# Performance work log

Hardware: AMD Instinct MI355X
Metric: run time of the kernel (lower is better)

The kernel has to match this reference:

```python
import jax, jax.numpy as jnp
import numpy as np

D = 1024      # n_embd
H = 16        # n_head
HD = D // H   # head_size = 64


def _layernorm(x, g, b, eps=1e-5):
    mu = jnp.mean(x, axis=-1, keepdims=True)
    var = jnp.mean((x - mu) ** 2, axis=-1, keepdims=True)
    return (x - mu) * jax.lax.rsqrt(var + eps) * g + b


def setup_inputs() -> dict:
    key = jax.random.key(0)
    ks = jax.random.split(key, 12)
    s = lambda fan_in: 1.0 / np.sqrt(fan_in)
    inp = {
        "x": jax.random.normal(ks[0], (4, 2048, D), dtype=jnp.float32),
        # attention projections (bias=False in Head), per-head weights fused into [D, D]
        "wq": jax.random.uniform(ks[1], (D, D), jnp.float32, -s(D), s(D)),
        "wk": jax.random.uniform(ks[2], (D, D), jnp.float32, -s(D), s(D)),
        "wv": jax.random.uniform(ks[3], (D, D), jnp.float32, -s(D), s(D)),
        "wo": jax.random.uniform(ks[4], (D, D), jnp.float32, -s(D), s(D)),
        "bo": jax.random.uniform(ks[5], (D,), jnp.float32, -s(D), s(D)),
        # feed-forward: D -> 4D -> D
        "w1": jax.random.uniform(ks[6], (D, 4 * D), jnp.float32, -s(D), s(D)),
        "b1": jax.random.uniform(ks[7], (4 * D,), jnp.float32, -s(D), s(D)),
        "w2": jax.random.uniform(ks[8], (4 * D, D), jnp.float32, -s(4 * D), s(4 * D)),
        "b2": jax.random.uniform(ks[9], (D,), jnp.float32, -s(4 * D), s(4 * D)),
        # layernorms
        "g_ln1": jnp.ones((D,), jnp.float32),
        "b_ln1": jnp.zeros((D,), jnp.float32),
        "g_ln2": jnp.ones((D,), jnp.float32),
        "b_ln2": jnp.zeros((D,), jnp.float32),
    }
    return inp


def reference(x, wq, wk, wv, wo, bo, w1, b1, w2, b2, g_ln1, b_ln1, g_ln2, b_ln2):
    B, T, _ = x.shape
    # --- self-attention on ln1(x) ---
    h = _layernorm(x, g_ln1, b_ln1)
    q = (h @ wq).reshape(B, T, H, HD)
    k = (h @ wk).reshape(B, T, H, HD)
    v = (h @ wv).reshape(B, T, H, HD)
    scores = jnp.einsum("bqhd,bkhd->bhqk", q, k) * (HD ** -0.5)
    causal = jnp.tril(jnp.ones((T, T), dtype=bool))
    scores = jnp.where(causal, scores, -jnp.inf)
    wei = jax.nn.softmax(scores, axis=-1)                    # [B,H,T,T]
    attn = jnp.einsum("bhqk,bkhd->bqhd", wei, v).reshape(B, T, D)
    x = x + attn @ wo + bo
    # --- feed-forward on ln2(x) ---
    h2 = _layernorm(x, g_ln2, b_ln2)
    x = x + jax.nn.relu(h2 @ w1 + b1) @ w2 + b2
    return x
```

## Files before the change

### kernel.cpp

```cpp
#include <hip/hip_runtime.h>
#include <cstdint>

typedef __bf16 bf16x8 __attribute__((ext_vector_type(8)));
typedef float f32x4 __attribute__((ext_vector_type(4)));
typedef unsigned int u32x4 __attribute__((ext_vector_type(4)));
typedef unsigned short u16x4 __attribute__((ext_vector_type(4)));

#define D_MODEL 1024
#define SEQ     2048
#define NBATCH  4
#define NHEAD   16
#define HDIM    64
#define NTOK    (NBATCH * SEQ)

__device__ __forceinline__ unsigned short f2bf(float f) {
  unsigned int u = __builtin_bit_cast(unsigned int, f);
  u += 0x7FFFu + ((u >> 16) & 1u);
  return (unsigned short)(u >> 16);
}

__device__ __forceinline__ bf16x8 load8bf(const unsigned short* p) {
  return __builtin_bit_cast(bf16x8, *(const u32x4*)p);
}

__device__ __forceinline__ f32x4 mfma16(bf16x8 a, bf16x8 b, f32x4 c) {
  return __builtin_amdgcn_mfma_f32_16x16x32_bf16(a, b, c, 0, 0, 0);
}

__device__ __forceinline__ void gload16(const unsigned short* g, unsigned short* l) {
  __builtin_amdgcn_global_load_lds((__attribute__((address_space(1))) void*)g,
                                   (__attribute__((address_space(3))) void*)l, 16, 0, 0);
}

__device__ __forceinline__ bf16x8 scale8(bf16x8 v, float s) {
  u32x4 u = __builtin_bit_cast(u32x4, v);
  unsigned short out[8];
  #pragma unroll
  for (int i = 0; i < 4; ++i) {
    unsigned int w = u[i];
    float lo = __builtin_bit_cast(float, w << 16) * s;
    float hi = __builtin_bit_cast(float, w & 0xFFFF0000u) * s;
    out[2 * i]     = f2bf(lo);
    out[2 * i + 1] = f2bf(hi);
  }
  return __builtin_bit_cast(bf16x8, *(u32x4*)out);
}

__global__ __launch_bounds__(256) void tcastT(const float* __restrict__ in,
                                              unsigned short* __restrict__ out,
                                              int K, int N) {
  __shared__ float tile[32][33];
  const int k0 = blockIdx.y * 32, n0 = blockIdx.x * 32;
  const int tx = threadIdx.x & 31, ty = threadIdx.x >> 5;
  #pragma unroll
  for (int j = 0; j < 4; ++j)
    tile[ty + 8 * j][tx] = in[(size_t)(k0 + ty + 8 * j) * N + n0 + tx];
  __syncthreads();
  #pragma unroll
  for (int j = 0; j < 4; ++j)
    out[(size_t)(n0 + ty + 8 * j) * K + k0 + tx] = f2bf(tile[tx][ty + 8 * j]);
}

__global__ __launch_bounds__(256) void ln_kernel(const float* __restrict__ x,
                                                 const float* __restrict__ g,
                                                 const float* __restrict__ bb,
                                                 unsigned short* __restrict__ out) {
  const int row = blockIdx.x, tid = threadIdx.x;
  const float4 xv = ((const float4*)(x + (size_t)row * D_MODEL))[tid];
  float s  = xv.x + xv.y + xv.z + xv.w;
  float ss = xv.x * xv.x + xv.y * xv.y + xv.z * xv.z + xv.w * xv.w;
  #pragma unroll
  for (int off = 1; off < 64; off <<= 1) { s += __shfl_xor(s, off); ss += __shfl_xor(ss, off); }
  __shared__ float red[8];
  const int wave = tid >> 6, lane = tid & 63;
  if (lane == 0) { red[wave] = s; red[4 + wave] = ss; }
  __syncthreads();
  s  = red[0] + red[1] + red[2] + red[3];
  ss = red[4] + red[5] + red[6] + red[7];
  const float mu   = s * (1.0f / D_MODEL);
  const float var  = ss * (1.0f / D_MODEL) - mu * mu;
  const float rstd = rsqrtf(var + 1e-5f);
  const float4 gv = ((const float4*)g)[tid];
  const float4 bv = ((const float4*)bb)[tid];
  u16x4 o;
  o.x = f2bf((xv.x - mu) * rstd * gv.x + bv.x);
  o.y = f2bf((xv.y - mu) * rstd * gv.y + bv.y);
  o.z = f2bf((xv.z - mu) * rstd * gv.z + bv.z);
  o.w = f2bf((xv.w - mu) * rstd * gv.w + bv.w);
  *(u16x4*)(out + (size_t)row * D_MODEL + tid * 4) = o;
}

template <bool BIAS, bool RELU, bool RES, bool OBF>
__global__ __launch_bounds__(256) void gemm_bt(const unsigned short* __restrict__ A,
                                               const unsigned short* __restrict__ Bt,
                                               const float* __restrict__ bias,
                                               const float* __restrict__ res,
                                               void* __restrict__ out,
                                               int M, int N, int K) {
  __shared__ __align__(16) unsigned short As[128 * 64];
  __shared__ __align__(16) unsigned short Bs[128 * 64];
  const int tid  = threadIdx.x;
  const int lin = blockIdx.y * gridDim.x + blockIdx.x;
  const int xcd = lin & 7, idx = lin >> 3;
  const int by = xcd * 8 + (idx & 7);
  const int bx = idx >> 3;
  const int row0 = by * 128, col0 = bx * 128;
  const int wave = tid >> 6, lane = tid & 63;
  const int wm = wave >> 1, wn = wave & 1;
  const int l15 = lane & 15, quad = lane >> 4;
  f32x4 acc[4][4] = {};

  const int tr = tid >> 3;
  const int tc = (tid & 7) ^ (tr & 7);
  const unsigned short* gA = A  + (size_t)(row0 + tr) * K + tc * 8;
  const unsigned short* gB = Bt + (size_t)(col0 + tr) * K + tc * 8;

  const int rowA = (wm * 64 + l15) * 64;
  const int rowB = (wn * 64 + l15) * 64;
  const int swz0 = (quad ^ (l15 & 7)) * 8;
  const int swz1 = ((4 + quad) ^ (l15 & 7)) * 8;

  for (int k0 = 0; k0 < K; k0 += 64) {
    #pragma unroll
    for (int i = 0; i < 4; ++i) {
      gload16(gA + (size_t)(i * 32) * K + k0, As + (i * 256 + tid) * 8);
      gload16(gB + (size_t)(i * 32) * K + k0, Bs + (i * 256 + tid) * 8);
    }
    __syncthreads();
    #pragma unroll
    for (int kf = 0; kf < 2; ++kf) {
      const int swz = kf ? swz1 : swz0;
      bf16x8 af[4], bfr[4];
      #pragma unroll
      for (int t = 0; t < 4; ++t) {
        af[t]  = load8bf(As + rowA + t * 1024 + swz);
        bfr[t] = load8bf(Bs + rowB + t * 1024 + swz);
      }
      #pragma unroll
      for (int i = 0; i < 4; ++i)
        #pragma unroll
        for (int j = 0; j < 4; ++j)
          acc[i][j] = mfma16(af[i], bfr[j], acc[i][j]);
    }
    __syncthreads();
  }

  const size_t rbase = (size_t)row0 + wm * 64 + quad * 4;
  const int cbase = col0 + wn * 64 + l15;
  #pragma unroll
  for (int i = 0; i < 4; ++i) {
    #pragma unroll
    for (int j = 0; j < 4; ++j) {
      const int col = cbase + j * 16;
      const float bval = BIAS ? bias[col] : 0.0f;
      #pragma unroll
      for (int r = 0; r < 4; ++r) {
        const size_t row = rbase + i * 16 + r;
        float v = acc[i][j][r];
        if (BIAS) v += bval;
        if (RELU) v = fmaxf(v, 0.0f);
        if (RES)  v += res[row * N + col];
        if (OBF)  ((unsigned short*)out)[row * N + col] = f2bf(v);
        else      ((float*)out)[row * N + col] = v;
      }
    }
  }
}

__global__ __launch_bounds__(256) void kvpack(const unsigned short* __restrict__ qkv,
                                              unsigned short* __restrict__ kp,
                                              unsigned short* __restrict__ vt) {
  const int t0 = blockIdx.x * 64;
  const int bh = blockIdx.y, b = bh >> 4, h = bh & 15;
  const int tid = threadIdx.x, lane = tid & 63, wave = tid >> 6;
  __shared__ __align__(16) unsigned short vstage[64 * 64];
  const size_t qbase = ((size_t)b * SEQ + t0) * 3072;
  #pragma unroll
  for (int i = 0; i < 2; ++i) {
    const int cid = i * 256 + tid;
    const int r = cid >> 3, c = cid & 7;
    u32x4 vv = *(const u32x4*)(qkv + qbase + (size_t)r * 3072 + 1024 + h * 64 + c * 8);
    *(u32x4*)(kp + ((size_t)bh * SEQ + t0 + r) * 64 + c * 8) = vv;
  }
  #pragma unroll
  for (int i = 0; i < 2; ++i) {
    const int cid = i * 256 + tid;
    const int r = cid >> 3, p = cid & 7, c = p ^ (r >> 3);
    gload16(qkv + qbase + (size_t)r * 3072 + 2048 + h * 64 + c * 8, vstage + cid * 8);
  }
  __syncthreads();
  #pragma unroll
  for (int it = 0; it < 2; ++it) {
    const int d = (lane & 7) + wave * 8 + it * 32;
    const int tc = lane >> 3;
    unsigned short tmp[8];
    #pragma unroll
    for (int j = 0; j < 8; ++j) {
      const int tj = tc * 8 + j;
      const int p = (d >> 3) ^ tc;
      tmp[j] = vstage[tj * 64 + p * 8 + (d & 7)];
    }
    *(u32x4*)(vt + ((size_t)bh * HDIM + d) * SEQ + t0 + tc * 8) = *(u32x4*)tmp;
  }
}

__global__ __launch_bounds__(256) void attn3(const unsigned short* __restrict__ qkv,
                                             const unsigned short* __restrict__ kp,
                                             const unsigned short* __restrict__ vt,
                                             unsigned short* __restrict__ attnb) {
  const int lin = (blockIdx.z * 16 + blockIdx.y) * 8 + blockIdx.x;
  const int xcd = lin & 7, idx = lin >> 3;
  const int bh = xcd * 8 + (idx >> 3);
  const int xb = idx & 7;
  const int b = bh >> 4, h = bh & 15;
  const int tid = threadIdx.x, wave = tid >> 6, lane = tid & 63;
  const int l15 = lane & 15, quad = lane >> 4;
  const size_t tokbase = (size_t)b * SEQ;

  __shared__ __align__(16) unsigned short ks[64 * 64];
  __shared__ __align__(16) unsigned short vts[64 * 64];
  __shared__ __align__(16) unsigned short plds[4][32 * 64];

  const unsigned short* kbase = kp + (size_t)bh * SEQ * HDIM;
  const unsigned short* vbase = vt + (size_t)bh * HDIM * SEQ;
  const float qscale = 0.18033688011112042f;

  for (int half = 0; half < 2; ++half) {
    const int qblk = (half == 0) ? (15 - xb) : xb;
    const int qw0 = qblk * 128 + wave * 32;

    bf16x8 qf[2][2];
    #pragma unroll
    for (int mf = 0; mf < 2; ++mf)
      #pragma unroll
      for (int kf = 0; kf < 2; ++kf)
        qf[mf][kf] = scale8(load8bf(qkv + (tokbase + qw0 + mf * 16 + l15) * 3072
                                    + h * HDIM + kf * 32 + quad * 8), qscale);

    f32x4 o[2][4] = {};
    float lsum[2][4] = {};

    const int ntiles = qblk * 2 + 2;
    for (int kt = 0; kt < ntiles; ++kt) {
      const int k0 = kt * 64;
      __syncthreads();
      #pragma unroll
      for (int i = 0; i < 2; ++i) {
        const int cid = i * 256 + tid;
        const int r = cid >> 3, p = cid & 7, c = p ^ (r & 7);
        gload16(kbase + (size_t)(k0 + r) * HDIM + c * 8, ks + cid * 8);
      }
      #pragma unroll
      for (int i = 0; i < 2; ++i) {
        const int cid = i * 256 + tid;
        const int d = cid >> 3, p = cid & 7, c = p ^ (d & 7);
        gload16(vbase + (size_t)d * SEQ + k0 + c * 8, vts + cid * 8);
      }
      __syncthreads();
      if (k0 <= qw0 + 31) {
        f32x4 s[2][4] = {};
        #pragma unroll
        for (int kf = 0; kf < 2; ++kf)
          #pragma unroll
          for (int nf = 0; nf < 4; ++nf) {
            const int row = nf * 16 + l15;
            const int p = (kf * 4 + quad) ^ (row & 7);
            const bf16x8 bk = load8bf(ks + row * 64 + p * 8);
            s[0][nf] = mfma16(qf[0][kf], bk, s[0][nf]);
            s[1][nf] = mfma16(qf[1][kf], bk, s[1][nf]);
          }
        #pragma unroll
        for (int mf = 0; mf < 2; ++mf)
          #pragma unroll
          for (int nf = 0; nf < 4; ++nf) {
            const int key = k0 + nf * 16 + l15;
            #pragma unroll
            for (int r = 0; r < 4; ++r) {
              const int lq = mf * 16 + quad * 4 + r;
              float p = __builtin_amdgcn_exp2f(s[mf][nf][r]);
              p = (key > qw0 + lq) ? 0.0f : p;
              const unsigned int pu = __builtin_bit_cast(unsigned int, p);
              lsum[mf][r] += __builtin_bit_cast(float, pu & 0xFFFF0000u);
              const int pc = ((nf * 16 + l15) >> 3) ^ (lq & 7) ^ ((lq >> 3) & 3);
              plds[wave][lq * 64 + pc * 8 + (l15 & 7)] = (unsigned short)(pu >> 16);
            }
          }
        __builtin_amdgcn_s_waitcnt(0);
        #pragma unroll
        for (int kf = 0; kf < 2; ++kf) {
          bf16x8 pa[2];
          #pragma unroll
          for (int mf = 0; mf < 2; ++mf) {
            const int lq = mf * 16 + l15;
            const int p = (kf * 4 + quad) ^ (lq & 7) ^ ((lq >> 3) & 3);
            pa[mf] = load8bf(&plds[wave][lq * 64 + p * 8]);
          }
          #pragma unroll
          for (int df = 0; df < 4; ++df) {
            const int row = df * 16 + l15;
            const int p = (kf * 4 + quad) ^ (row & 7);
            const bf16x8 vb = load8bf(vts + row * 64 + p * 8);
            o[0][df] = mfma16(pa[0], vb, o[0][df]);
            o[1][df] = mfma16(pa[1], vb, o[1][df]);
          }
        }
      }
    }
    #pragma unroll
    for (int mf = 0; mf < 2; ++mf)
      #pragma unroll
      for (int r = 0; r < 4; ++r) {
        float l = lsum[mf][r];
        #pragma unroll
        for (int off = 1; off < 16; off <<= 1) l += __shfl_xor(l, off);
        const float rl = 1.0f / l;
        const size_t row = tokbase + qw0 + mf * 16 + quad * 4 + r;
        #pragma unroll
        for (int df = 0; df < 4; ++df)
          attnb[row * D_MODEL + h * HDIM + df * 16 + l15] = f2bf(o[mf][df][r] * rl);
      }
  }
}

extern "C" void kernel_launch(void* const* d_in, const int* in_sizes, int n_in,
                              void* d_out, int out_size, void* d_ws, size_t ws_size,
                              hipStream_t stream) {
  const float* x    = (const float*)d_in[0];
  const float* wq   = (const float*)d_in[1];
  const float* wk   = (const float*)d_in[2];
  const float* wv   = (const float*)d_in[3];
  const float* wo   = (const float*)d_in[4];
  const float* bo   = (const float*)d_in[5];
  const float* w1   = (const float*)d_in[6];
  const float* b1   = (const float*)d_in[7];
  const float* w2   = (const float*)d_in[8];
  const float* b2   = (const float*)d_in[9];
  const float* g1   = (const float*)d_in[10];
  const float* bl1  = (const float*)d_in[11];
  const float* g2   = (const float*)d_in[12];
  const float* bl2  = (const float*)d_in[13];
  float* out = (float*)d_out;

  char* ws = (char*)d_ws;
  size_t off = 0;
  auto alloc = [&](size_t bytes) { char* p = ws + off; off += (bytes + 255) & ~(size_t)255; return p; };
  unsigned short* wqkv_t = (unsigned short*)alloc((size_t)3072 * 1024 * 2);
  unsigned short* wo_t   = (unsigned short*)alloc((size_t)1024 * 1024 * 2);
  unsigned short* w1_t   = (unsigned short*)alloc((size_t)4096 * 1024 * 2);
  unsigned short* w2_t   = (unsigned short*)alloc((size_t)1024 * 4096 * 2);
  unsigned short* h1     = (unsigned short*)alloc((size_t)NTOK * 1024 * 2);
  unsigned short* qkv    = (unsigned short*)alloc((size_t)NTOK * 3072 * 2);
  unsigned short* attnb  = (unsigned short*)alloc((size_t)NTOK * 1024 * 2);
  unsigned short* h2     = (unsigned short*)alloc((size_t)NTOK * 1024 * 2);
  unsigned short* ffn1   = (unsigned short*)alloc((size_t)NTOK * 4096 * 2);
  unsigned short* kpb = h1;
  unsigned short* vtb = h2;

  tcastT<<<dim3(32, 32), 256, 0, stream>>>(wq, wqkv_t,               1024, 1024);
  tcastT<<<dim3(32, 32), 256, 0, stream>>>(wk, wqkv_t + 1024 * 1024, 1024, 1024);
  tcastT<<<dim3(32, 32), 256, 0, stream>>>(wv, wqkv_t + 2048 * 1024, 1024, 1024);
  tcastT<<<dim3(32, 32), 256, 0, stream>>>(wo, wo_t,                 1024, 1024);
  tcastT<<<dim3(128, 32), 256, 0, stream>>>(w1, w1_t, 1024, 4096);
  tcastT<<<dim3(32, 128), 256, 0, stream>>>(w2, w2_t, 4096, 1024);

  ln_kernel<<<NTOK, 256, 0, stream>>>(x, g1, bl1, h1);
  gemm_bt<false, false, false, true><<<dim3(24, 64), 256, 0, stream>>>(
      h1, wqkv_t, nullptr, nullptr, qkv, NTOK, 3072, 1024);
  kvpack<<<dim3(SEQ / 64, NBATCH * NHEAD), 256, 0, stream>>>(qkv, kpb, vtb);
  attn3<<<dim3(SEQ / 256, NHEAD, NBATCH), 256, 0, stream>>>(qkv, kpb, vtb, attnb);
  gemm_bt<true, false, true, false><<<dim3(8, 64), 256, 0, stream>>>(
      attnb, wo_t, bo, x, out, NTOK, 1024, 1024);
  ln_kernel<<<NTOK, 256, 0, stream>>>(out, g2, bl2, h2);
  gemm_bt<true, true, false, true><<<dim3(32, 64), 256, 0, stream>>>(
      h2, w1_t, b1, nullptr, ffn1, NTOK, 4096, 1024);
  gemm_bt<true, false, true, false><<<dim3(8, 64), 256, 0, stream>>>(
      ffn1, w2_t, b2, out, out, NTOK, 1024, 4096);
  (void)in_sizes; (void)n_in; (void)out_size; (void)ws_size;
}
```

Before: 515.3 us.

## Fuse K/V packing and Q scaling into QKV GEMM epilogue; merge weight casts

After: 479.4 us. 7.0% less time.

```diff
diff --git a/kernel.cpp b/kernel.cpp
--- a/kernel.cpp
+++ b/kernel.cpp
@@ -12,6 +12,7 @@
 #define NHEAD   16
 #define HDIM    64
 #define NTOK    (NBATCH * SEQ)
+#define QSCALE  0.18033688011112042f
 
 __device__ __forceinline__ unsigned short f2bf(float f) {
   unsigned int u = __builtin_bit_cast(unsigned int, f);
@@ -32,25 +33,33 @@
                                    (__attribute__((address_space(3))) void*)l, 16, 0, 0);
 }
 
-__device__ __forceinline__ bf16x8 scale8(bf16x8 v, float s) {
-  u32x4 u = __builtin_bit_cast(u32x4, v);
-  unsigned short out[8];
-  #pragma unroll
-  for (int i = 0; i < 4; ++i) {
-    unsigned int w = u[i];
-    float lo = __builtin_bit_cast(float, w << 16) * s;
-    float hi = __builtin_bit_cast(float, w & 0xFFFF0000u) * s;
-    out[2 * i]     = f2bf(lo);
-    out[2 * i + 1] = f2bf(hi);
+__global__ __launch_bounds__(256) void tcast_all(const float* __restrict__ wq,
+                                                 const float* __restrict__ wk,
+                                                 const float* __restrict__ wv,
+                                                 const float* __restrict__ wo,
+                                                 const float* __restrict__ w1,
+                                                 const float* __restrict__ w2,
+                                                 unsigned short* __restrict__ wqkv_t,
+                                                 unsigned short* __restrict__ wo_t,
+                                                 unsigned short* __restrict__ w1_t,
+                                                 unsigned short* __restrict__ w2_t) {
+  const int id = blockIdx.x;
+  const float* in; unsigned short* out; int K, N, k0, n0;
+  if (id < 4096) {
+    const int seg = id >> 10, r = id & 1023;
+    in  = seg == 0 ? wq : seg == 1 ? wk : seg == 2 ? wv : wo;
+    out = seg == 3 ? wo_t : wqkv_t + (size_t)seg * 1024 * 1024;
+    K = 1024; N = 1024; n0 = (r & 31) * 32; k0 = (r >> 5) * 32;
+  } else if (id < 8192) {
+    const int r = id - 4096;
+    in = w1; out = w1_t; K = 1024; N = 4096;
+    n0 = (r & 127) * 32; k0 = (r >> 7) * 32;
+  } else {
+    const int r = id - 8192;
+    in = w2; out = w2_t; K = 4096; N = 1024;
+    n0 = (r & 31) * 32; k0 = (r >> 5) * 32;
   }
-  return __builtin_bit_cast(bf16x8, *(u32x4*)out);
-}
-
-__global__ __launch_bounds__(256) void tcastT(const float* __restrict__ in,
-                                              unsigned short* __restrict__ out,
-                                              int K, int N) {
   __shared__ float tile[32][33];
-  const int k0 = blockIdx.y * 32, n0 = blockIdx.x * 32;
   const int tx = threadIdx.x & 31, ty = threadIdx.x >> 5;
   #pragma unroll
   for (int j = 0; j < 4; ++j)
@@ -90,12 +99,15 @@
   *(u16x4*)(out + (size_t)row * D_MODEL + tid * 4) = o;
 }
 
-template <bool BIAS, bool RELU, bool RES, bool OBF>
+template <bool BIAS, bool RELU, bool RES, bool OBF, bool QKV>
 __global__ __launch_bounds__(256) void gemm_bt(const unsigned short* __restrict__ A,
                                                const unsigned short* __restrict__ Bt,
                                                const float* __restrict__ bias,
                                                const float* __restrict__ res,
                                                void* __restrict__ out,
+                                               unsigned short* __restrict__ qb,
+                                               unsigned short* __restrict__ kp,
+                                               unsigned short* __restrict__ vt,
                                                int M, int N, int K) {
   __shared__ __align__(16) unsigned short As[128 * 64];
   __shared__ __align__(16) unsigned short Bs[128 * 64];
@@ -147,64 +159,61 @@
 
   const size_t rbase = (size_t)row0 + wm * 64 + quad * 4;
   const int cbase = col0 + wn * 64 + l15;
-  #pragma unroll
-  for (int i = 0; i < 4; ++i) {
-    #pragma unroll
-    for (int j = 0; j < 4; ++j) {
-      const int col = cbase + j * 16;
-      const float bval = BIAS ? bias[col] : 0.0f;
-      #pragma unroll
-      for (int r = 0; r < 4; ++r) {
-        const size_t row = rbase + i * 16 + r;
-        float v = acc[i][j][r];
-        if (BIAS) v += bval;
-        if (RELU) v = fmaxf(v, 0.0f);
-        if (RES)  v += res[row * N + col];
-        if (OBF)  ((unsigned short*)out)[row * N + col] = f2bf(v);
-        else      ((float*)out)[row * N + col] = v;
+  if (QKV) {
+    const int sec = col0 >> 10;
+    #pragma unroll
+    for (int i = 0; i < 4; ++i) {
+      #pragma unroll
+      for (int j = 0; j < 4; ++j) {
+        const int col = cbase + j * 16;
+        if (sec == 0) {
+          #pragma unroll
+          for (int r = 0; r < 4; ++r) {
+            const size_t row = rbase + i * 16 + r;
+            qb[row * 1024 + col] = f2bf(acc[i][j][r] * QSCALE);
+          }
+        } else if (sec == 1) {
+          const int c2 = col - 1024, hh = c2 >> 6, d = c2 & 63;
+          #pragma unroll
+          for (int r = 0; r < 4; ++r) {
+            const size_t row = rbase + i * 16 + r;
+            const int bb = (int)(row >> 11), t = (int)(row & 2047);
+            kp[(((size_t)(bb * 16 + hh)) * SEQ + t) * 64 + d] = f2bf(acc[i][j][r]);
+          }
+        } else {
+          const int c2 = col - 2048, hh = c2 >> 6, d = c2 & 63;
+          const size_t t0 = rbase + i * 16;
+          const int bb = (int)(t0 >> 11);
+          u16x4 pk;
+          #pragma unroll
+          for (int r = 0; r < 4; ++r) pk[r] = f2bf(acc[i][j][r]);
+          *(u16x4*)(vt + ((size_t)(bb * 16 + hh) * 64 + d) * SEQ + (t0 & 2047)) = pk;
+        }
+      }
+    }
+  } else {
+    #pragma unroll
+    for (int i = 0; i < 4; ++i) {
+      #pragma unroll
+      for (int j = 0; j < 4; ++j) {
+        const int col = cbase + j * 16;
+        const float bval = BIAS ? bias[col] : 0.0f;
+        #pragma unroll
+        for (int r = 0; r < 4; ++r) {
+          const size_t row = rbase + i * 16 + r;
+          float v = acc[i][j][r];
+          if (BIAS) v += bval;
+          if (RELU) v = fmaxf(v, 0.0f);
+          if (RES)  v += res[row * N + col];
+          if (OBF)  ((unsigned short*)out)[row * N + col] = f2bf(v);
+          else      ((float*)out)[row * N + col] = v;
+        }
       }
     }
   }
 }
 
-__global__ __launch_bounds__(256) void kvpack(const unsigned short* __restrict__ qkv,
-                                              unsigned short* __restrict__ kp,
-                                              unsigned short* __restrict__ vt) {
-  const int t0 = blockIdx.x * 64;
-  const int bh = blockIdx.y, b = bh >> 4, h = bh & 15;
-  const int tid = threadIdx.x, lane = tid & 63, wave = tid >> 6;
-  __shared__ __align__(16) unsigned short vstage[64 * 64];
-  const size_t qbase = ((size_t)b * SEQ + t0) * 3072;
-  #pragma unroll
-  for (int i = 0; i < 2; ++i) {
-    const int cid = i * 256 + tid;
-    const int r = cid >> 3, c = cid & 7;
-    u32x4 vv = *(const u32x4*)(qkv + qbase + (size_t)r * 3072 + 1024 + h * 64 + c * 8);
-    *(u32x4*)(kp + ((size_t)bh * SEQ + t0 + r) * 64 + c * 8) = vv;
-  }
-  #pragma unroll
-  for (int i = 0; i < 2; ++i) {
-    const int cid = i * 256 + tid;
-    const int r = cid >> 3, p = cid & 7, c = p ^ (r >> 3);
-    gload16(qkv + qbase + (size_t)r * 3072 + 2048 + h * 64 + c * 8, vstage + cid * 8);
-  }
-  __syncthreads();
-  #pragma unroll
-  for (int it = 0; it < 2; ++it) {
-    const int d = (lane & 7) + wave * 8 + it * 32;
-    const int tc = lane >> 3;
-    unsigned short tmp[8];
-    #pragma unroll
-    for (int j = 0; j < 8; ++j) {
-      const int tj = tc * 8 + j;
-      const int p = (d >> 3) ^ tc;
-      tmp[j] = vstage[tj * 64 + p * 8 + (d & 7)];
-    }
-    *(u32x4*)(vt + ((size_t)bh * HDIM + d) * SEQ + t0 + tc * 8) = *(u32x4*)tmp;
-  }
-}
-
-__global__ __launch_bounds__(256) void attn3(const unsigned short* __restrict__ qkv,
+__global__ __launch_bounds__(256) void attn4(const unsigned short* __restrict__ qb,
                                              const unsigned short* __restrict__ kp,
                                              const unsigned short* __restrict__ vt,
                                              unsigned short* __restrict__ attnb) {
@@ -223,7 +232,6 @@
 
   const unsigned short* kbase = kp + (size_t)bh * SEQ * HDIM;
   const unsigned short* vbase = vt + (size_t)bh * HDIM * SEQ;
-  const float qscale = 0.18033688011112042f;
 
   for (int half = 0; half < 2; ++half) {
     const int qblk = (half == 0) ? (15 - xb) : xb;
@@ -234,8 +242,8 @@
     for (int mf = 0; mf < 2; ++mf)
       #pragma unroll
       for (int kf = 0; kf < 2; ++kf)
-        qf[mf][kf] = scale8(load8bf(qkv + (tokbase + qw0 + mf * 16 + l15) * 3072
-                                    + h * HDIM + kf * 32 + quad * 8), qscale);
+        qf[mf][kf] = load8bf(qb + (tokbase + qw0 + mf * 16 + l15) * 1024
+                             + h * HDIM + kf * 32 + quad * 8);
 
     f32x4 o[2][4] = {};
     float lsum[2][4] = {};
@@ -349,31 +357,25 @@
   unsigned short* w1_t   = (unsigned short*)alloc((size_t)4096 * 1024 * 2);
   unsigned short* w2_t   = (unsigned short*)alloc((size_t)1024 * 4096 * 2);
   unsigned short* h1     = (unsigned short*)alloc((size_t)NTOK * 1024 * 2);
-  unsigned short* qkv    = (unsigned short*)alloc((size_t)NTOK * 3072 * 2);
+  unsigned short* kpb    = (unsigned short*)alloc((size_t)NTOK * 1024 * 2);
+  unsigned short* vtb    = (unsigned short*)alloc((size_t)NTOK * 1024 * 2);
   unsigned short* attnb  = (unsigned short*)alloc((size_t)NTOK * 1024 * 2);
   unsigned short* h2     = (unsigned short*)alloc((size_t)NTOK * 1024 * 2);
   unsigned short* ffn1   = (unsigned short*)alloc((size_t)NTOK * 4096 * 2);
-  unsigned short* kpb = h1;
-  unsigned short* vtb = h2;
-
-  tcastT<<<dim3(32, 32), 256, 0, stream>>>(wq, wqkv_t,               1024, 1024);
-  tcastT<<<dim3(32, 32), 256, 0, stream>>>(wk, wqkv_t + 1024 * 1024, 1024, 1024);
-  tcastT<<<dim3(32, 32), 256, 0, stream>>>(wv, wqkv_t + 2048 * 1024, 1024, 1024);
-  tcastT<<<dim3(32, 32), 256, 0, stream>>>(wo, wo_t,                 1024, 1024);
-  tcastT<<<dim3(128, 32), 256, 0, stream>>>(w1, w1_t, 1024, 4096);
-  tcastT<<<dim3(32, 128), 256, 0, stream>>>(w2, w2_t, 4096, 1024);
-
+  unsigned short* qb = attnb;
+
+  tcast_all<<<12288, 256, 0, stream>>>(wq, wk, wv, wo, w1, w2,
+                                       wqkv_t, wo_t, w1_t, w2_t);
   ln_kernel<<<NTOK, 256, 0, stream>>>(x, g1, bl1, h1);
-  gemm_bt<false, false, false, true><<<dim3(24, 64), 256, 0, stream>>>(
-      h1, wqkv_t, nullptr, nullptr, qkv, NTOK, 3072, 1024);
-  kvpack<<<dim3(SEQ / 64, NBATCH * NHEAD), 256, 0, stream>>>(qkv, kpb, vtb);
-  attn3<<<dim3(SEQ / 256, NHEAD, NBATCH), 256, 0, stream>>>(qkv, kpb, vtb, attnb);
-  gemm_bt<true, false, true, false><<<dim3(8, 64), 256, 0, stream>>>(
-      attnb, wo_t, bo, x, out, NTOK, 1024, 1024);
+  gemm_bt<false, false, false, true, true><<<dim3(24, 64), 256, 0, stream>>>(
+      h1, wqkv_t, nullptr, nullptr, nullptr, qb, kpb, vtb, NTOK, 3072, 1024);
+  attn4<<<dim3(SEQ / 256, NHEAD, NBATCH), 256, 0, stream>>>(qb, kpb, vtb, attnb);
+  gemm_bt<true, false, true, false, false><<<dim3(8, 64), 256, 0, stream>>>(
+      attnb, wo_t, bo, x, out, nullptr, nullptr, nullptr, NTOK, 1024, 1024);
   ln_kernel<<<NTOK, 256, 0, stream>>>(out, g2, bl2, h2);
-  gemm_bt<true, true, false, true><<<dim3(32, 64), 256, 0, stream>>>(
-      h2, w1_t, b1, nullptr, ffn1, NTOK, 4096, 1024);
-  gemm_bt<true, false, true, false><<<dim3(8, 64), 256, 0, stream>>>(
-      ffn1, w2_t, b2, out, out, NTOK, 1024, 4096);
+  gemm_bt<true, true, false, true, false><<<dim3(32, 64), 256, 0, stream>>>(
+      h2, w1_t, b1, nullptr, ffn1, nullptr, nullptr, nullptr, NTOK, 4096, 1024);
+  gemm_bt<true, false, true, false, false><<<dim3(8, 64), 256, 0, stream>>>(
+      ffn1, w2_t, b2, out, out, nullptr, nullptr, nullptr, NTOK, 1024, 4096);
   (void)in_sizes; (void)n_in; (void)out_size; (void)ws_size;
 }
```
